# Kernel optimization log

Measured on AMD Instinct MI355X. Metric: run time of the kernel, lower is better.

Reference implementation:

```python
import jax, jax.numpy as jnp
import numpy as np

N_NODES = 100000
N_EDGES = 1600000
D_IN = 128
D_HID = 64


def setup_inputs() -> dict:
    key = jax.random.key(0)
    k1, k2, k3, k4 = jax.random.split(key, 4)
    x = jax.random.normal(k1, (N_NODES, D_IN), dtype=jnp.float32)
    edge_index = jax.random.randint(k2, (2, N_EDGES), 0, N_NODES, dtype=jnp.int64)
    W1 = jax.random.normal(k3, (D_IN, D_HID), dtype=jnp.float32) / np.sqrt(D_IN)
    b1 = jnp.zeros((D_HID,), dtype=jnp.float32)
    W2 = jax.random.normal(k4, (D_HID, 1), dtype=jnp.float32) / np.sqrt(D_HID)
    b2 = jnp.zeros((1,), dtype=jnp.float32)
    return {"x": x, "edge_index": edge_index, "W1": W1, "b1": b1, "W2": W2, "b2": b2}


def _gcn_layer(x, W, b, src, dst, norm, n):
    # PyG GCNConv: linear transform, then normalized scatter-add aggregation, then bias
    h = x @ W                                   # [N, d_out]
    msg = h[src] * norm[:, None]                # gather + edge-weight   [E', d_out]
    out = jax.ops.segment_sum(msg, dst, num_segments=n)  # scatter-add
    return out + b


def reference(x, edge_index, W1, b1, W2, b2):
    n = x.shape[0]
    loops = jnp.arange(n, dtype=edge_index.dtype)
    src = jnp.concatenate([edge_index[0], loops])  # self-loops added (GCN default)
    dst = jnp.concatenate([edge_index[1], loops])
    # symmetric normalization: deg^{-1/2}[src] * deg^{-1/2}[dst]
    deg = jax.ops.segment_sum(jnp.ones(dst.shape, x.dtype), dst, num_segments=n)
    dis = jnp.where(deg > 0, jax.lax.rsqrt(jnp.maximum(deg, 1e-12)), 0.0)
    norm = dis[src] * dis[dst]
    h = jax.nn.relu(_gcn_layer(x, W1, b1, src, dst, norm, n))
    y = _gcn_layer(h, W2, b2, src, dst, norm, n)   # [N, 1]
    # ConstantPad1d((0, num_node_features-1), 0) -> [N, D_IN]
    return jnp.pad(y, ((0, 0), (0, x.shape[1] - 1)))
```

## Files before the change

kernel.cpp:

```cpp
#include <hip/hip_runtime.h>

#define N_NODES 100000
#define N_EDGES 1600000
#define D_IN 128
#define D_HID 64

#define BKT_SHIFT 8
#define BKT_NODES 256
#define NB 391
#define NBLK 392
#define SLOT 32
#define SEG4 (SLOT / 4)
#define REG4 (NBLK * SEG4)
#define BKT_CAP 5120
#define OVF_CAP 8192

typedef __attribute__((ext_vector_type(8))) short bf16x8;
typedef __attribute__((ext_vector_type(4))) float f32x4;

__device__ __forceinline__ unsigned short f2b(float f) {
    union { float f; unsigned u; } c; c.f = f;
    unsigned r = (c.u + 0x7FFFu + ((c.u >> 16) & 1u)) >> 16;
    return (unsigned short)r;
}
__device__ __forceinline__ float blo(unsigned u) { return __uint_as_float(u << 16); }
__device__ __forceinline__ float bhi(unsigned u) { return __uint_as_float(u & 0xffff0000u); }

__global__ __launch_bounds__(256) void k_prep(const float* __restrict__ W1,
                                              unsigned short* __restrict__ w1t,
                                              int* __restrict__ ovf_cnt) {
    int t = blockIdx.x * 256 + threadIdx.x;
    if (t == 0) ovf_cnt[0] = 0;
    int k = t >> 6, f = t & 63;
    w1t[f * D_IN + k] = f2b(W1[t]);
}

__global__ __launch_bounds__(256) void k_escatter(const int* __restrict__ src,
                                                  const int* __restrict__ dst,
                                                  int* __restrict__ pairs,
                                                  int* __restrict__ cnt_blk,
                                                  int* __restrict__ ovf_cnt,
                                                  int2* __restrict__ ovf, int E) {
    __shared__ int lcur[NB];
    int tid = threadIdx.x;
    for (int t = tid; t < NB; t += 256) lcur[t] = 0;
    __syncthreads();
    int chunk = (E + NBLK - 1) / NBLK;
    int beg = blockIdx.x * chunk;
    int end = min(beg + chunk, E);
    for (int e = beg + tid; e < end; e += 256) {
        int d = dst[e], s = src[e];
        int bk = d >> BKT_SHIFT;
        int slot = atomicAdd(&lcur[bk], 1);
        if (slot < SLOT)
            pairs[(bk * NBLK + blockIdx.x) * SLOT + slot] = (s << BKT_SHIFT) | (d & (BKT_NODES - 1));
        else {
            int o = atomicAdd(ovf_cnt, 1);
            if (o < OVF_CAP) ovf[o] = make_int2(s, d);
        }
    }
    __syncthreads();
    for (int t = tid; t < NB; t += 256)
        cnt_blk[t * NBLK + blockIdx.x] = min(lcur[t], SLOT);
}

__global__ __launch_bounds__(256) void k_bsort(const uint4* __restrict__ pairs4,
                                               const int* __restrict__ cnt_blk,
                                               const int* __restrict__ ovf_cnt,
                                               const int2* __restrict__ ovf,
                                               int* __restrict__ srcs_sorted,
                                               int* __restrict__ row_start,
                                               int* __restrict__ row_end,
                                               float* __restrict__ dis, int n) {
    __shared__ int segc[NBLK];
    __shared__ int cnt[BKT_NODES];
    __shared__ int exc[BKT_NODES];
    __shared__ int sorted[BKT_CAP];
    __shared__ int nE_sh;
    int b = blockIdx.x;
    int tid = threadIdx.x;
    int node0 = b << BKT_SHIFT;
    int ocnt = min(ovf_cnt[0], OVF_CAP);
    const uint4* region = pairs4 + (size_t)b * REG4;

    for (int i = tid; i < NBLK; i += 256) segc[i] = cnt_blk[b * NBLK + i];
    cnt[tid] = 0;
    __syncthreads();

    for (int i4 = tid; i4 < REG4; i4 += 256) {
        uint4 v = region[i4];
        int c = segc[i4 >> 3];
        int k = (i4 & 7) * 4;
        if (k < c)     atomicAdd(&cnt[v.x & (BKT_NODES - 1)], 1);
        if (k + 1 < c) atomicAdd(&cnt[v.y & (BKT_NODES - 1)], 1);
        if (k + 2 < c) atomicAdd(&cnt[v.z & (BKT_NODES - 1)], 1);
        if (k + 3 < c) atomicAdd(&cnt[v.w & (BKT_NODES - 1)], 1);
    }
    for (int k = tid; k < ocnt; k += 256) {
        int2 e = ovf[k];
        if ((e.y >> BKT_SHIFT) == b) atomicAdd(&cnt[e.y & (BKT_NODES - 1)], 1);
    }
    __syncthreads();

    if (tid < 64) {
        int run = 0;
        for (int c = 0; c < BKT_NODES; c += 64) {
            int v = cnt[c + tid];
            int inc = v;
            for (int off = 1; off < 64; off <<= 1) {
                int t2 = __shfl_up(inc, off);
                if (tid >= off) inc += t2;
            }
            exc[c + tid] = run + inc - v;
            run += __shfl(inc, 63);
        }
        if (tid == 63) nE_sh = run;
    }
    __syncthreads();

    int node = node0 + tid;
    if (node < n) {
        int rs = b * BKT_CAP + exc[tid];
        row_start[node] = rs;
        row_end[node] = rs + cnt[tid];
        dis[node] = rsqrtf((float)cnt[tid] + 1.0f);
    }
    int nE = nE_sh;
    __syncthreads();
    cnt[tid] = exc[tid];
    __syncthreads();

    for (int i4 = tid; i4 < REG4; i4 += 256) {
        uint4 v = region[i4];
        int c = segc[i4 >> 3];
        int k = (i4 & 7) * 4;
        if (k < c)     { int p = atomicAdd(&cnt[v.x & (BKT_NODES - 1)], 1); sorted[p] = v.x >> BKT_SHIFT; }
        if (k + 1 < c) { int p = atomicAdd(&cnt[v.y & (BKT_NODES - 1)], 1); sorted[p] = v.y >> BKT_SHIFT; }
        if (k + 2 < c) { int p = atomicAdd(&cnt[v.z & (BKT_NODES - 1)], 1); sorted[p] = v.z >> BKT_SHIFT; }
        if (k + 3 < c) { int p = atomicAdd(&cnt[v.w & (BKT_NODES - 1)], 1); sorted[p] = v.w >> BKT_SHIFT; }
    }
    for (int k = tid; k < ocnt; k += 256) {
        int2 e = ovf[k];
        if ((e.y >> BKT_SHIFT) == b) {
            int p = atomicAdd(&cnt[e.y & (BKT_NODES - 1)], 1);
            sorted[p] = e.x;
        }
    }
    __syncthreads();

    int gbase = b * BKT_CAP;
    for (int k = tid; k < nE; k += 256)
        srcs_sorted[gbase + k] = sorted[k];
}

#define LS 136
__global__ __launch_bounds__(256) void k_gemm1(const float* __restrict__ x,
                                               const uint4* __restrict__ w1t4,
                                               const float* __restrict__ dis,
                                               unsigned short* __restrict__ h1s, int n) {
    __shared__ unsigned short xs[64 * LS];
    __shared__ unsigned short ws[64 * LS];
    int tid = threadIdx.x;
    int node0 = blockIdx.x * 64;

#pragma unroll
    for (int it = 0; it < 4; ++it) {
        int e = tid + it * 256;
        int f = e >> 4, c = e & 15;
        *(uint4*)&ws[f * LS + c * 8] = w1t4[e];
    }
#pragma unroll
    for (int it = 0; it < 8; ++it) {
        int e4 = tid + it * 256;
        int node = e4 >> 5;
        int k = (e4 & 31) * 4;
        float4 v = make_float4(0.f, 0.f, 0.f, 0.f);
        if (node0 + node < n)
            v = ((const float4*)x)[((size_t)(node0 + node) * D_IN + k) >> 2];
        uint2 u;
        u.x = (unsigned)f2b(v.x) | ((unsigned)f2b(v.y) << 16);
        u.y = (unsigned)f2b(v.z) | ((unsigned)f2b(v.w) << 16);
        *(uint2*)&xs[node * LS + k] = u;
    }
    __syncthreads();

    int wv = tid >> 6;
    int lane = tid & 63;
    int m16 = lane & 15;
    int q = lane >> 4;

    bf16x8 afrag[4];
#pragma unroll
    for (int ks = 0; ks < 4; ++ks)
        afrag[ks] = *(const bf16x8*)&xs[(wv * 16 + m16) * LS + ks * 32 + q * 8];

    f32x4 acc[4];
#pragma unroll
    for (int ft = 0; ft < 4; ++ft) acc[ft] = (f32x4){0.f, 0.f, 0.f, 0.f};

#pragma unroll
    for (int ft = 0; ft < 4; ++ft)
#pragma unroll
        for (int ks = 0; ks < 4; ++ks) {
            bf16x8 bfrag = *(const bf16x8*)&ws[(ft * 16 + m16) * LS + ks * 32 + q * 8];
            acc[ft] = __builtin_amdgcn_mfma_f32_16x16x32_bf16(afrag[ks], bfrag, acc[ft], 0, 0, 0);
        }

#pragma unroll
    for (int r = 0; r < 4; ++r) {
        int node = node0 + wv * 16 + q * 4 + r;
        if (node < n) {
            float d = dis[node];
#pragma unroll
            for (int ft = 0; ft < 4; ++ft)
                h1s[(size_t)node * D_HID + ft * 16 + m16] = f2b(acc[ft][r] * d);
        }
    }
}

__global__ __launch_bounds__(256) void k_gather1(const int* __restrict__ srcs,
                                                 const int* __restrict__ row_start,
                                                 const int* __restrict__ row_end,
                                                 const float* __restrict__ dis,
                                                 const uint4* __restrict__ h4,
                                                 const float* __restrict__ b1,
                                                 const float* __restrict__ W2,
                                                 float* __restrict__ zd, int n) {
    int i = blockIdx.x * 8 + (threadIdx.x >> 5);
    int lane = threadIdx.x & 63;
    int g = (lane >> 3) & 3;
    int m8 = lane & 7;
    float dd = dis[i];

    float a0, a1, a2, a3, a4, a5, a6, a7;
    {
        uint4 u = h4[(unsigned)i * 8u + m8];
        float w = (g == 0) ? 1.f : 0.f;
        a0 = w * blo(u.x); a1 = w * bhi(u.x);
        a2 = w * blo(u.y); a3 = w * bhi(u.y);
        a4 = w * blo(u.z); a5 = w * bhi(u.z);
        a6 = w * blo(u.w); a7 = w * bhi(u.w);
    }

#define ACC(u) { a0 += blo(u.x); a1 += bhi(u.x); a2 += blo(u.y); a3 += bhi(u.y); \
                 a4 += blo(u.z); a5 += bhi(u.z); a6 += blo(u.w); a7 += bhi(u.w); }
    int end = row_end[i];
    int j = row_start[i] + g;
    for (; j + 4 < end; j += 8) {
        int s0 = srcs[j];
        int s1 = srcs[j + 4];
        uint4 u0 = h4[(unsigned)s0 * 8u + m8];
        uint4 u1 = h4[(unsigned)s1 * 8u + m8];
        ACC(u0); ACC(u1);
    }
    if (j < end) {
        int s0 = srcs[j];
        uint4 u0 = h4[(unsigned)s0 * 8u + m8];
        ACC(u0);
    }
#undef ACC

#pragma unroll
    for (int off = 8; off < 32; off <<= 1) {
        a0 += __shfl_xor(a0, off); a1 += __shfl_xor(a1, off);
        a2 += __shfl_xor(a2, off); a3 += __shfl_xor(a3, off);
        a4 += __shfl_xor(a4, off); a5 += __shfl_xor(a5, off);
        a6 += __shfl_xor(a6, off); a7 += __shfl_xor(a7, off);
    }
    float4 ba = ((const float4*)b1)[m8 * 2];
    float4 bb = ((const float4*)b1)[m8 * 2 + 1];
    float4 wa = ((const float4*)W2)[m8 * 2];
    float4 wb = ((const float4*)W2)[m8 * 2 + 1];
    float v = fmaxf(fmaf(dd, a0, ba.x), 0.f) * wa.x + fmaxf(fmaf(dd, a1, ba.y), 0.f) * wa.y
            + fmaxf(fmaf(dd, a2, ba.z), 0.f) * wa.z + fmaxf(fmaf(dd, a3, ba.w), 0.f) * wa.w
            + fmaxf(fmaf(dd, a4, bb.x), 0.f) * wb.x + fmaxf(fmaf(dd, a5, bb.y), 0.f) * wb.y
            + fmaxf(fmaf(dd, a6, bb.z), 0.f) * wb.z + fmaxf(fmaf(dd, a7, bb.w), 0.f) * wb.w;
#pragma unroll
    for (int off = 1; off < 8; off <<= 1) v += __shfl_xor(v, off);
    if ((lane & 31) == 0) zd[i] = v * dd;
}

__global__ __launch_bounds__(256) void k_gather2(const int* __restrict__ srcs,
                                                 const int* __restrict__ row_start,
                                                 const int* __restrict__ row_end,
                                                 const float* __restrict__ dis,
                                                 const float* __restrict__ zd,
                                                 const float* __restrict__ b2,
                                                 float* __restrict__ out, int n) {
    int i = blockIdx.x * 8 + (threadIdx.x >> 5);
    int l = threadIdx.x & 31;
    float acc = 0.f;
    int beg = row_start[i], end = row_end[i];
    for (int j = beg + l; j < end; j += 32)
        acc += zd[srcs[j]];
#pragma unroll
    for (int off = 1; off < 32; off <<= 1) acc += __shfl_xor(acc, off);
    float y = (acc + zd[i]) * dis[i] + b2[0];
    float4 v = make_float4(0.f, 0.f, 0.f, 0.f);
    if (l == 0) v.x = y;
    ((float4*)out)[(size_t)i * 32 + l] = v;
}

extern "C" void kernel_launch(void* const* d_in, const int* in_sizes, int n_in,
                              void* d_out, int out_size, void* d_ws, size_t ws_size,
                              hipStream_t stream) {
    const float* x  = (const float*)d_in[0];
    const int*   ei = (const int*)d_in[1];
    const float* W1 = (const float*)d_in[2];
    const float* b1 = (const float*)d_in[3];
    const float* W2 = (const float*)d_in[4];
    const float* b2 = (const float*)d_in[5];
    float* out = (float*)d_out;

    const int n = N_NODES;
    const int E = N_EDGES;
    const int* src = ei;
    const int* dst = ei + E;

    int* pairs       = (int*)d_ws;
    int* cnt_blk     = pairs + (size_t)NB * NBLK * SLOT;
    int* srcs_sorted = cnt_blk + (size_t)NB * NBLK;
    int* row_start   = srcs_sorted + (size_t)NB * BKT_CAP;
    int* row_end     = row_start + n;
    int* ovf_cnt     = row_end + n;
    int2* ovf        = (int2*)(ovf_cnt + 4);
    float* dis       = (float*)(ovf + OVF_CAP);
    unsigned short* h1s = (unsigned short*)(dis + n);
    unsigned short* w1t = h1s + (size_t)n * D_HID;
    float* zd        = (float*)(w1t + D_IN * D_HID);

    k_prep<<<32, 256, 0, stream>>>(W1, w1t, ovf_cnt);
    k_escatter<<<NBLK, 256, 0, stream>>>(src, dst, pairs, cnt_blk, ovf_cnt, ovf, E);
    k_bsort<<<NB, 256, 0, stream>>>((const uint4*)pairs, cnt_blk, ovf_cnt, ovf,
                                    srcs_sorted, row_start, row_end, dis, n);

    k_gemm1<<<(n + 63) / 64, 256, 0, stream>>>(x, (const uint4*)w1t, dis, h1s, n);

    k_gather1<<<(n + 7) / 8, 256, 0, stream>>>(srcs_sorted, row_start, row_end, dis,
                                               (const uint4*)h1s, b1, W2, zd, n);
    k_gather2<<<(n + 7) / 8, 256, 0, stream>>>(srcs_sorted, row_start, row_end, dis,
                                               zd, b2, out, n);
}
```

Before: 212.7 us.

## Give each node a full wavefront in gather1 with prefetched indices; enlarge sort blocks

The layer-1 gather now assigns one 64-lane wavefront per node instead of half a wave. The wave loads up to 64 neighbour indices in a single coalesced read, broadcasts them with shuffles, and issues four independent row loads per lane so more memory requests are in flight. The edge-scatter and bucket-sort kernels are launched with 512 and 1024 threads, with guards added for the per-node shared arrays. Nodes with low degree now leave more lanes idle, and the larger sort blocks may lower occupancy or increase shared-atomic contention.

```diff
diff --git a/kernel.cpp b/kernel.cpp
--- a/kernel.cpp
+++ b/kernel.cpp
@@ -15,6 +15,9 @@
 #define BKT_CAP 5120
 #define OVF_CAP 8192
 
+#define EST 512
+#define BST 1024
+
 typedef __attribute__((ext_vector_type(8))) short bf16x8;
 typedef __attribute__((ext_vector_type(4))) float f32x4;
 
@@ -35,7 +38,7 @@
     w1t[f * D_IN + k] = f2b(W1[t]);
 }
 
-__global__ __launch_bounds__(256) void k_escatter(const int* __restrict__ src,
+__global__ __launch_bounds__(EST) void k_escatter(const int* __restrict__ src,
                                                   const int* __restrict__ dst,
                                                   int* __restrict__ pairs,
                                                   int* __restrict__ cnt_blk,
@@ -43,12 +46,12 @@
                                                   int2* __restrict__ ovf, int E) {
     __shared__ int lcur[NB];
     int tid = threadIdx.x;
-    for (int t = tid; t < NB; t += 256) lcur[t] = 0;
+    for (int t = tid; t < NB; t += EST) lcur[t] = 0;
     __syncthreads();
     int chunk = (E + NBLK - 1) / NBLK;
     int beg = blockIdx.x * chunk;
     int end = min(beg + chunk, E);
-    for (int e = beg + tid; e < end; e += 256) {
+    for (int e = beg + tid; e < end; e += EST) {
         int d = dst[e], s = src[e];
         int bk = d >> BKT_SHIFT;
         int slot = atomicAdd(&lcur[bk], 1);
@@ -60,11 +63,11 @@
         }
     }
     __syncthreads();
-    for (int t = tid; t < NB; t += 256)
+    for (int t = tid; t < NB; t += EST)
         cnt_blk[t * NBLK + blockIdx.x] = min(lcur[t], SLOT);
 }
 
-__global__ __launch_bounds__(256) void k_bsort(const uint4* __restrict__ pairs4,
+__global__ __launch_bounds__(BST) void k_bsort(const uint4* __restrict__ pairs4,
                                                const int* __restrict__ cnt_blk,
                                                const int* __restrict__ ovf_cnt,
                                                const int2* __restrict__ ovf,
@@ -83,11 +86,11 @@
     int ocnt = min(ovf_cnt[0], OVF_CAP);
     const uint4* region = pairs4 + (size_t)b * REG4;
 
-    for (int i = tid; i < NBLK; i += 256) segc[i] = cnt_blk[b * NBLK + i];
-    cnt[tid] = 0;
-    __syncthreads();
-
-    for (int i4 = tid; i4 < REG4; i4 += 256) {
+    for (int i = tid; i < NBLK; i += BST) segc[i] = cnt_blk[b * NBLK + i];
+    if (tid < BKT_NODES) cnt[tid] = 0;
+    __syncthreads();
+
+    for (int i4 = tid; i4 < REG4; i4 += BST) {
         uint4 v = region[i4];
         int c = segc[i4 >> 3];
         int k = (i4 & 7) * 4;
@@ -96,7 +99,7 @@
         if (k + 2 < c) atomicAdd(&cnt[v.z & (BKT_NODES - 1)], 1);
         if (k + 3 < c) atomicAdd(&cnt[v.w & (BKT_NODES - 1)], 1);
     }
-    for (int k = tid; k < ocnt; k += 256) {
+    for (int k = tid; k < ocnt; k += BST) {
         int2 e = ovf[k];
         if ((e.y >> BKT_SHIFT) == b) atomicAdd(&cnt[e.y & (BKT_NODES - 1)], 1);
     }
@@ -118,19 +121,21 @@
     }
     __syncthreads();
 
-    int node = node0 + tid;
-    if (node < n) {
-        int rs = b * BKT_CAP + exc[tid];
-        row_start[node] = rs;
-        row_end[node] = rs + cnt[tid];
-        dis[node] = rsqrtf((float)cnt[tid] + 1.0f);
+    if (tid < BKT_NODES) {
+        int node = node0 + tid;
+        if (node < n) {
+            int rs = b * BKT_CAP + exc[tid];
+            row_start[node] = rs;
+            row_end[node] = rs + cnt[tid];
+            dis[node] = rsqrtf((float)cnt[tid] + 1.0f);
+        }
     }
     int nE = nE_sh;
     __syncthreads();
-    cnt[tid] = exc[tid];
-    __syncthreads();
-
-    for (int i4 = tid; i4 < REG4; i4 += 256) {
+    if (tid < BKT_NODES) cnt[tid] = exc[tid];
+    __syncthreads();
+
+    for (int i4 = tid; i4 < REG4; i4 += BST) {
         uint4 v = region[i4];
         int c = segc[i4 >> 3];
         int k = (i4 & 7) * 4;
@@ -139,7 +144,7 @@
         if (k + 2 < c) { int p = atomicAdd(&cnt[v.z & (BKT_NODES - 1)], 1); sorted[p] = v.z >> BKT_SHIFT; }
         if (k + 3 < c) { int p = atomicAdd(&cnt[v.w & (BKT_NODES - 1)], 1); sorted[p] = v.w >> BKT_SHIFT; }
     }
-    for (int k = tid; k < ocnt; k += 256) {
+    for (int k = tid; k < ocnt; k += BST) {
         int2 e = ovf[k];
         if ((e.y >> BKT_SHIFT) == b) {
             int p = atomicAdd(&cnt[e.y & (BKT_NODES - 1)], 1);
@@ -149,7 +154,7 @@
     __syncthreads();
 
     int gbase = b * BKT_CAP;
-    for (int k = tid; k < nE; k += 256)
+    for (int k = tid; k < nE; k += BST)
         srcs_sorted[gbase + k] = sorted[k];
 }
 
@@ -226,11 +231,13 @@
                                                  const float* __restrict__ b1,
                                                  const float* __restrict__ W2,
                                                  float* __restrict__ zd, int n) {
-    int i = blockIdx.x * 8 + (threadIdx.x >> 5);
+    int i = blockIdx.x * 4 + (threadIdx.x >> 6);
     int lane = threadIdx.x & 63;
-    int g = (lane >> 3) & 3;
+    int g = lane >> 3;
     int m8 = lane & 7;
     float dd = dis[i];
+    int beg = row_start[i];
+    int deg = row_end[i] - beg;
 
     float a0, a1, a2, a3, a4, a5, a6, a7;
     {
@@ -242,26 +249,48 @@
         a6 = w * blo(u.w); a7 = w * bhi(u.w);
     }
 
+    int s_pre = 0;
+    if (lane < deg) s_pre = srcs[beg + lane];
+    int dmax = min(deg, 64);
+
 #define ACC(u) { a0 += blo(u.x); a1 += bhi(u.x); a2 += blo(u.y); a3 += bhi(u.y); \
                  a4 += blo(u.z); a5 += bhi(u.z); a6 += blo(u.w); a7 += bhi(u.w); }
-    int end = row_end[i];
-    int j = row_start[i] + g;
-    for (; j + 4 < end; j += 8) {
-        int s0 = srcs[j];
-        int s1 = srcs[j + 4];
-        uint4 u0 = h4[(unsigned)s0 * 8u + m8];
-        uint4 u1 = h4[(unsigned)s1 * 8u + m8];
-        ACC(u0); ACC(u1);
-    }
-    if (j < end) {
-        int s0 = srcs[j];
-        uint4 u0 = h4[(unsigned)s0 * 8u + m8];
-        ACC(u0);
+
+    {
+        int k0 = g, k1 = g + 8, k2 = g + 16, k3 = g + 24;
+        int s0 = __shfl(s_pre, k0), s1 = __shfl(s_pre, k1),
+            s2 = __shfl(s_pre, k2), s3 = __shfl(s_pre, k3);
+        uint4 u0 = h4[(unsigned)(k0 < dmax ? s0 : (int)i) * 8u + m8];
+        uint4 u1 = h4[(unsigned)(k1 < dmax ? s1 : (int)i) * 8u + m8];
+        uint4 u2 = h4[(unsigned)(k2 < dmax ? s2 : (int)i) * 8u + m8];
+        uint4 u3 = h4[(unsigned)(k3 < dmax ? s3 : (int)i) * 8u + m8];
+        if (k0 < dmax) ACC(u0);
+        if (k1 < dmax) ACC(u1);
+        if (k2 < dmax) ACC(u2);
+        if (k3 < dmax) ACC(u3);
+    }
+    if (deg > 32) {
+        int k0 = g + 32, k1 = g + 40, k2 = g + 48, k3 = g + 56;
+        int s0 = __shfl(s_pre, k0), s1 = __shfl(s_pre, k1),
+            s2 = __shfl(s_pre, k2), s3 = __shfl(s_pre, k3);
+        uint4 u0 = h4[(unsigned)(k0 < dmax ? s0 : (int)i) * 8u + m8];
+        uint4 u1 = h4[(unsigned)(k1 < dmax ? s1 : (int)i) * 8u + m8];
+        uint4 u2 = h4[(unsigned)(k2 < dmax ? s2 : (int)i) * 8u + m8];
+        uint4 u3 = h4[(unsigned)(k3 < dmax ? s3 : (int)i) * 8u + m8];
+        if (k0 < dmax) ACC(u0);
+        if (k1 < dmax) ACC(u1);
+        if (k2 < dmax) ACC(u2);
+        if (k3 < dmax) ACC(u3);
+    }
+    for (int k = 64 + g; k < deg; k += 8) {
+        int s = srcs[beg + k];
+        uint4 u = h4[(unsigned)s * 8u + m8];
+        ACC(u);
     }
 #undef ACC
 
 #pragma unroll
-    for (int off = 8; off < 32; off <<= 1) {
+    for (int off = 8; off < 64; off <<= 1) {
         a0 += __shfl_xor(a0, off); a1 += __shfl_xor(a1, off);
         a2 += __shfl_xor(a2, off); a3 += __shfl_xor(a3, off);
         a4 += __shfl_xor(a4, off); a5 += __shfl_xor(a5, off);
@@ -277,7 +306,7 @@
             + fmaxf(fmaf(dd, a6, bb.z), 0.f) * wb.z + fmaxf(fmaf(dd, a7, bb.w), 0.f) * wb.w;
 #pragma unroll
     for (int off = 1; off < 8; off <<= 1) v += __shfl_xor(v, off);
-    if ((lane & 31) == 0) zd[i] = v * dd;
+    if (lane == 0) zd[i] = v * dd;
 }
 
 __global__ __launch_bounds__(256) void k_gather2(const int* __restrict__ srcs,
@@ -330,13 +359,13 @@
     float* zd        = (float*)(w1t + D_IN * D_HID);
 
     k_prep<<<32, 256, 0, stream>>>(W1, w1t, ovf_cnt);
-    k_escatter<<<NBLK, 256, 0, stream>>>(src, dst, pairs, cnt_blk, ovf_cnt, ovf, E);
-    k_bsort<<<NB, 256, 0, stream>>>((const uint4*)pairs, cnt_blk, ovf_cnt, ovf,
+    k_escatter<<<NBLK, EST, 0, stream>>>(src, dst, pairs, cnt_blk, ovf_cnt, ovf, E);
+    k_bsort<<<NB, BST, 0, stream>>>((const uint4*)pairs, cnt_blk, ovf_cnt, ovf,
                                     srcs_sorted, row_start, row_end, dis, n);
 
     k_gemm1<<<(n + 63) / 64, 256, 0, stream>>>(x, (const uint4*)w1t, dis, h1s, n);
 
-    k_gather1<<<(n + 7) / 8, 256, 0, stream>>>(srcs_sorted, row_start, row_end, dis,
+    k_gather1<<<(n + 3) / 4, 256, 0, stream>>>(srcs_sorted, row_start, row_end, dis,
                                                (const uint4*)h1s, b1, W2, zd, n);
     k_gather2<<<(n + 7) / 8, 256, 0, stream>>>(srcs_sorted, row_start, row_end, dis,
                                                zd, b2, out, n);
```

New measurement: 207.4 us. 1.03x faster.
